# Kernel tuning notes

Hardware: AMD Instinct MI355X
Metric: run time of the kernel (lower is better)

## Reference

```python
import jax, jax.numpy as jnp
import numpy as np

N = 16384          # total nodes (128 graphs x 128 ops)
G = 128            # number of graphs
NPG = N // G       # nodes per graph
DIN = 64           # op_input_dim
H = 64             # hidden_dim
BN_EPS = 1e-5


def setup_inputs() -> dict:
    key = jax.random.key(0)
    ks = jax.random.split(key, 16)
    x = jax.random.normal(ks[0], (N, DIN), dtype=jnp.float32)
    # sparse-ish 0/1 adjacency stored dense (as torch.mm path expects); add self-loops so degrees > 0
    u = jax.random.uniform(ks[1], (N, N), dtype=jnp.float32)
    adj = jnp.maximum((u < 0.004).astype(jnp.float32), jnp.eye(N, dtype=jnp.float32))
    # graph_pool: [G, N] average-pooling matrix (block rows of 1/NPG)
    rows = jnp.repeat(jnp.arange(G), NPG)
    graph_pool = jnp.zeros((G, N), jnp.float32).at[rows, jnp.arange(N)].set(1.0 / NPG)
    s = 0.05
    params = {}
    dims_in = [DIN, H]
    for l in range(2):
        d_in = dims_in[l]
        params[f"W1_{l}"] = jax.random.normal(ks[2 + 6 * l], (d_in, H), jnp.float32) * s
        params[f"b1_{l}"] = jnp.zeros((H,), jnp.float32)
        params[f"g1_{l}"] = jnp.ones((H,), jnp.float32)
        params[f"be1_{l}"] = jnp.zeros((H,), jnp.float32)
        params[f"W2_{l}"] = jax.random.normal(ks[3 + 6 * l], (H, H), jnp.float32) * s
        params[f"b2_{l}"] = jnp.zeros((H,), jnp.float32)
        params[f"g_{l}"] = jnp.ones((H,), jnp.float32)   # outer BN gamma
        params[f"be_{l}"] = jnp.zeros((H,), jnp.float32)  # outer BN beta
    return {"x": x, "adj": adj, "graph_pool": graph_pool, **params}


def _bn(h, g, b):
    # training-mode BatchNorm1d over node axis (biased var), eps=1e-5
    m = jnp.mean(h, axis=0)
    v = jnp.var(h, axis=0)
    return g * (h - m) * jax.lax.rsqrt(v + BN_EPS) + b


def _mlp(h, W1, b1, g1, be1, W2, b2):
    # 2-layer MLP: Linear -> BN -> ReLU -> Linear
    return jax.nn.relu(_bn(h @ W1 + b1, g1, be1)) @ W2 + b2


def reference(x, adj, graph_pool,
              W1_0, b1_0, g1_0, be1_0, W2_0, b2_0, g_0, be_0,
              W1_1, b1_1, g1_1, be1_1, W2_1, b2_1, g_1, be_1):
    deg = adj @ jnp.ones((adj.shape[0], 1), adj.dtype)  # [N,1]
    h = x
    layers = [
        (W1_0, b1_0, g1_0, be1_0, W2_0, b2_0, g_0, be_0),
        (W1_1, b1_1, g1_1, be1_1, W2_1, b2_1, g_1, be_1),
    ]
    for (W1, b1, g1, be1, W2, b2, g, be) in layers:
        pooled = (adj @ h) / deg                 # average neighbor aggregation
        pooled_rep = _mlp(pooled, W1, b1, g1, be1, W2, b2)
        h = jax.nn.relu(_bn(pooled_rep, g, be))
    h_nodes = h
    pooled_h = graph_pool @ h                    # [G, H] graph readout
    return (pooled_h, h_nodes)
```

## Files before the change

### kernel.cpp

```cpp
#include <hip/hip_runtime.h>
#include <hip/hip_bf16.h>
#include <stdint.h>

#define N_NODES 16384
#define GG      128
#define HD      64
#define MAXD    192
#define BN_EPS  1e-5f

typedef unsigned short u16;
typedef unsigned int   u32;
typedef unsigned long long u64;
typedef u32 u32x4 __attribute__((ext_vector_type(4)));

__device__ __forceinline__ float bf2f(u16 u) {
    union { u32 i; float f; } c; c.i = ((u32)u) << 16; return c.f;
}
__device__ __forceinline__ float ldp(const void* p, int i, int flag) {
    return flag ? ((const float*)p)[i] : bf2f(((const u16*)p)[i]);
}

__global__ __launch_bounds__(256) void k_scan_gather(
    const void* __restrict__ adjv, const void* __restrict__ xv,
    u16* __restrict__ cols, int* __restrict__ cnt,
    float* __restrict__ invdeg, float* __restrict__ pooled,
    double* __restrict__ statsD, int* __restrict__ flagp)
{
    __shared__ __align__(16) u16 sc[4][MAXD];
    const int wave = threadIdx.x >> 6, lane = threadIdx.x & 63;
    const int row = blockIdx.x * 4 + wave;
    const u32 w0 = *(const u32*)adjv;
    const int flag = ((w0 & 0xFFFFu) == 0) ? 1 : 0;
    const u64 ltmask = ((1ull << lane) - 1ull);

    const int gid = blockIdx.x * 256 + threadIdx.x;
    if (gid < 512) statsD[gid] = 0.0;
    if (gid == 0) *flagp = flag;

    u16* __restrict__ srow = sc[wave];
    int base = 0;
    if (flag) {
        const u32x4* __restrict__ arow =
            (const u32x4*)((const u32*)adjv + (size_t)row * N_NODES) + lane;
        u32x4 p0 = __builtin_nontemporal_load(arow);
        u32x4 p1 = __builtin_nontemporal_load(arow + 64);
        for (int c = 0; c < N_NODES; c += 256) {
            u32x4 raw = p0;
            p0 = p1;
            if (c + 512 < N_NODES)
                p1 = __builtin_nontemporal_load(arow + (c + 512) / 4);
            #pragma unroll
            for (int e = 0; e < 4; ++e) {
                u32 w = raw[e];
                u64 m = __ballot(w != 0);
                if (m) {
                    if (w) {
                        int p = base + __popcll(m & ltmask);
                        if (p < MAXD) srow[p] = (u16)(c + lane * 4 + e);
                    }
                    base += __popcll(m);
                }
            }
        }
    } else {
        const u32x4* __restrict__ arow =
            (const u32x4*)((const u16*)adjv + (size_t)row * N_NODES) + lane;
        u32x4 p0 = __builtin_nontemporal_load(arow);
        u32x4 p1 = __builtin_nontemporal_load(arow + 64);
        for (int c = 0; c < N_NODES; c += 512) {
            u32x4 raw = p0;
            p0 = p1;
            if (c + 1024 < N_NODES)
                p1 = __builtin_nontemporal_load(arow + (c + 1024) / 8);
            #pragma unroll
            for (int e = 0; e < 8; ++e) {
                u16 u = (u16)(raw[e >> 1] >> ((e & 1) * 16));
                u64 m = __ballot(u != 0);
                if (m) {
                    if (u) {
                        int p = base + __popcll(m & ltmask);
                        if (p < MAXD) srow[p] = (u16)(c + lane * 8 + e);
                    }
                    base += __popcll(m);
                }
            }
        }
    }
    const int n = (base < MAXD) ? base : MAXD;
    if (lane == 0) cnt[row] = n;
    __syncthreads();

    {
        u32* __restrict__ crow32 = (u32*)(cols + (size_t)row * MAXD);
        const u32* __restrict__ s32 = (const u32*)srow;
        #pragma unroll
        for (int t = lane; t < MAXD / 2; t += 64) crow32[t] = s32[t];
    }

    float acc = 0.f;
    int k = 0;
    if (flag) {
        const float* __restrict__ x = (const float*)xv;
        for (; k + 4 <= n; k += 4) {
            ushort4 j4 = *(const ushort4*)&srow[k];
            float v0 = x[(size_t)j4.x * HD + lane];
            float v1 = x[(size_t)j4.y * HD + lane];
            float v2 = x[(size_t)j4.z * HD + lane];
            float v3 = x[(size_t)j4.w * HD + lane];
            acc += (v0 + v1) + (v2 + v3);
        }
        for (; k < n; ++k) acc += x[(size_t)srow[k] * HD + lane];
    } else {
        const u16* __restrict__ x = (const u16*)xv;
        for (; k + 4 <= n; k += 4) {
            ushort4 j4 = *(const ushort4*)&srow[k];
            float v0 = bf2f(x[(size_t)j4.x * HD + lane]);
            float v1 = bf2f(x[(size_t)j4.y * HD + lane]);
            float v2 = bf2f(x[(size_t)j4.z * HD + lane]);
            float v3 = bf2f(x[(size_t)j4.w * HD + lane]);
            acc += (v0 + v1) + (v2 + v3);
        }
        for (; k < n; ++k) acc += bf2f(x[(size_t)srow[k] * HD + lane]);
    }
    float inv = 1.f / (float)n;
    pooled[(size_t)row * HD + lane] = acc * inv;
    if (lane == 0) invdeg[row] = inv;
}

template<bool AFFINE>
__global__ __launch_bounds__(256) void k_mm(
    const float* __restrict__ src, const double* __restrict__ stats,
    const void* __restrict__ g, const void* __restrict__ be,
    const void* __restrict__ W, const void* __restrict__ bias,
    float* __restrict__ dst, const int* __restrict__ flagp)
{
    __shared__ float Wf[64 * 64];
    __shared__ float S[16 * 64];
    __shared__ float ac[128];
    const int tid = threadIdx.x;
    const int flag = *flagp;
    if (AFFINE) {
        if (tid < 64) {
            double m = stats[tid] * (1.0 / N_NODES);
            double v = stats[64 + tid] * (1.0 / N_NODES) - m * m;
            float A = ldp(g, tid, flag) / sqrtf((float)v + BN_EPS);
            ac[tid] = A;
            ac[64 + tid] = ldp(be, tid, flag) - (float)m * A;
        }
        __syncthreads();
    }
    for (int i = tid; i < 64 * 64; i += 256) Wf[i] = ldp(W, i, flag);
    const int rbase = blockIdx.x * 16;
    {
        float4 v = *(const float4*)&src[(size_t)rbase * 64 + tid * 4];
        if (AFFINE) {
            const int f0 = (tid * 4) & 63;
            v.x = fmaxf(fmaf(ac[f0 + 0], v.x, ac[64 + f0 + 0]), 0.f);
            v.y = fmaxf(fmaf(ac[f0 + 1], v.y, ac[64 + f0 + 1]), 0.f);
            v.z = fmaxf(fmaf(ac[f0 + 2], v.z, ac[64 + f0 + 2]), 0.f);
            v.w = fmaxf(fmaf(ac[f0 + 3], v.w, ac[64 + f0 + 3]), 0.f);
        }
        *(float4*)&S[tid * 4] = v;
    }
    __syncthreads();
    const int f = tid & 63, r0 = (tid >> 6) * 4;
    const float b = ldp(bias, f, flag);
    float a0 = b, a1 = b, a2 = b, a3 = b;
    #pragma unroll
    for (int k = 0; k < 64; ++k) {
        const float wk = Wf[k * 64 + f];
        a0 = fmaf(S[(r0 + 0) * 64 + k], wk, a0);
        a1 = fmaf(S[(r0 + 1) * 64 + k], wk, a1);
        a2 = fmaf(S[(r0 + 2) * 64 + k], wk, a2);
        a3 = fmaf(S[(r0 + 3) * 64 + k], wk, a3);
    }
    dst[(size_t)(rbase + r0 + 0) * 64 + f] = a0;
    dst[(size_t)(rbase + r0 + 1) * 64 + f] = a1;
    dst[(size_t)(rbase + r0 + 2) * 64 + f] = a2;
    dst[(size_t)(rbase + r0 + 3) * 64 + f] = a3;
}

__global__ __launch_bounds__(256) void k_stats(
    const float* __restrict__ src, double* __restrict__ statsOut)
{
    __shared__ double shs[256];
    __shared__ double shq[256];
    const int tid = threadIdx.x;
    const int f = tid & 63, rsub = tid >> 6;
    const int rbase = blockIdx.x * 64;
    double s = 0.0, q = 0.0;
    for (int r = rsub; r < 64; r += 4) {
        float v = src[(size_t)(rbase + r) * 64 + f];
        s += (double)v;
        q += (double)v * (double)v;
    }
    shs[tid] = s; shq[tid] = q;
    __syncthreads();
    if (tid < 64) {
        double S = shs[tid] + shs[64 + tid] + shs[128 + tid] + shs[192 + tid];
        double Q = shq[tid] + shq[64 + tid] + shq[128 + tid] + shq[192 + tid];
        atomicAdd(&statsOut[tid], S);
        atomicAdd(&statsOut[64 + tid], Q);
    }
}

__global__ __launch_bounds__(256) void k_bnrelu(
    const float* __restrict__ src, const double* __restrict__ stats,
    const void* __restrict__ g, const void* __restrict__ be,
    float* __restrict__ dst, const int* __restrict__ flagp)
{
    __shared__ float ac[128];
    const int tid = threadIdx.x;
    const int flag = *flagp;
    if (tid < 64) {
        double m = stats[tid] * (1.0 / N_NODES);
        double v = stats[64 + tid] * (1.0 / N_NODES) - m * m;
        float A = ldp(g, tid, flag) / sqrtf((float)v + BN_EPS);
        ac[tid] = A;
        ac[64 + tid] = ldp(be, tid, flag) - (float)m * A;
    }
    __syncthreads();
    const size_t idx = ((size_t)blockIdx.x * 256 + tid) * 4;
    const int f0 = (int)(idx & 63);
    float4 t = *(const float4*)&src[idx];
    const float4 A4 = *(const float4*)&ac[f0];
    const float4 C4 = *(const float4*)&ac[64 + f0];
    float4 r;
    r.x = fmaxf(fmaf(A4.x, t.x, C4.x), 0.f);
    r.y = fmaxf(fmaf(A4.y, t.y, C4.y), 0.f);
    r.z = fmaxf(fmaf(A4.z, t.z, C4.z), 0.f);
    r.w = fmaxf(fmaf(A4.w, t.w, C4.w), 0.f);
    *(float4*)&dst[idx] = r;
}

__global__ __launch_bounds__(256) void k_spmm(
    const float* __restrict__ t, const double* __restrict__ stats,
    const void* __restrict__ g, const void* __restrict__ be,
    const u16* __restrict__ cols, const int* __restrict__ cnt,
    const float* __restrict__ invdeg, float* __restrict__ pooled,
    const int* __restrict__ flagp)
{
    const int wave = threadIdx.x >> 6, lane = threadIdx.x & 63;
    const int row = blockIdx.x * 4 + wave;
    const int flag = *flagp;
    double md = stats[lane] * (1.0 / N_NODES);
    double vd = stats[64 + lane] * (1.0 / N_NODES) - md * md;
    const float A = ldp(g, lane, flag) / sqrtf((float)vd + BN_EPS);
    const float C = ldp(be, lane, flag) - (float)md * A;

    const u16* __restrict__ crow = cols + (size_t)row * MAXD;
    const int n = cnt[row];
    float acc = 0.f;
    int k = 0;
    for (; k + 4 <= n; k += 4) {
        ushort4 j4 = *(const ushort4*)&crow[k];
        float v0 = t[(size_t)j4.x * HD + lane];
        float v1 = t[(size_t)j4.y * HD + lane];
        float v2 = t[(size_t)j4.z * HD + lane];
        float v3 = t[(size_t)j4.w * HD + lane];
        acc += fmaxf(fmaf(A, v0, C), 0.f);
        acc += fmaxf(fmaf(A, v1, C), 0.f);
        acc += fmaxf(fmaf(A, v2, C), 0.f);
        acc += fmaxf(fmaf(A, v3, C), 0.f);
    }
    for (; k < n; ++k) {
        float vv = t[(size_t)crow[k] * HD + lane];
        acc += fmaxf(fmaf(A, vv, C), 0.f);
    }
    pooled[(size_t)row * HD + lane] = acc * invdeg[row];
}

__global__ __launch_bounds__(1024) void k_pool(
    const void* __restrict__ gpv, const float* __restrict__ h,
    float* __restrict__ out, const int* __restrict__ flagp)
{
    __shared__ float red[16 * 64];
    const int g = blockIdx.x;
    const int wave = threadIdx.x >> 6, lane = threadIdx.x & 63;
    const int flag = *flagp;
    float acc = 0.f;
    const int jb0 = wave * (N_NODES / 16);
    if (flag) {
        const float* __restrict__ grow = (const float*)gpv + (size_t)g * N_NODES;
        for (int jb = jb0; jb < jb0 + N_NODES / 16; jb += 4) {
            float4 raw = *(const float4*)(grow + jb);
            if (raw.x != 0.f) acc += raw.x * h[(size_t)(jb + 0) * HD + lane];
            if (raw.y != 0.f) acc += raw.y * h[(size_t)(jb + 1) * HD + lane];
            if (raw.z != 0.f) acc += raw.z * h[(size_t)(jb + 2) * HD + lane];
            if (raw.w != 0.f) acc += raw.w * h[(size_t)(jb + 3) * HD + lane];
        }
    } else {
        const u16* __restrict__ grow = (const u16*)gpv + (size_t)g * N_NODES;
        for (int jb = jb0; jb < jb0 + N_NODES / 16; jb += 8) {
            uint4 raw = *(const uint4*)(grow + jb);
            const u32 w[4] = {raw.x, raw.y, raw.z, raw.w};
            #pragma unroll
            for (int e = 0; e < 8; ++e) {
                u16 u = (u16)(w[e >> 1] >> ((e & 1) * 16));
                if (u) acc += bf2f(u) * h[(size_t)(jb + e) * HD + lane];
            }
        }
    }
    red[wave * 64 + lane] = acc;
    __syncthreads();
    if (wave == 0) {
        float s = 0.f;
        #pragma unroll
        for (int w2 = 0; w2 < 16; ++w2) s += red[w2 * 64 + lane];
        out[g * 64 + lane] = s;
    }
}

extern "C" void kernel_launch(void* const* d_in, const int* in_sizes, int n_in,
                              void* d_out, int out_size, void* d_ws, size_t ws_size,
                              hipStream_t stream)
{
    const void* x    = d_in[0];
    const void* adj  = d_in[1];
    const void* gp   = d_in[2];
    const void* W1_0 = d_in[3];
    const void* b1_0 = d_in[4];
    const void* g1_0 = d_in[5];
    const void* be1_0= d_in[6];
    const void* W2_0 = d_in[7];
    const void* b2_0 = d_in[8];
    const void* g_0  = d_in[9];
    const void* be_0 = d_in[10];
    const void* W1_1 = d_in[11];
    const void* b1_1 = d_in[12];
    const void* g1_1 = d_in[13];
    const void* be1_1= d_in[14];
    const void* W2_1 = d_in[15];
    const void* b2_1 = d_in[16];
    const void* g_1  = d_in[17];
    const void* be_1 = d_in[18];

    char* ws = (char*)d_ws;
    float*  P      = (float*) (ws);
    float*  A      = (float*) (ws + (4u  << 20));
    float*  B      = (float*) (ws + (8u  << 20));
    u16*    cols   = (u16*)   (ws + (12u << 20));
    int*    cnt    = (int*)   (ws + (18u << 20));
    float*  invdeg = (float*) (ws + (18u << 20) + 65536);
    double* sd     = (double*)(ws + (18u << 20) + 131072);
    int*    flag   = (int*)   (ws + (18u << 20) + 131072 + 4096);

    float* out_pool  = (float*)d_out;
    float* out_nodes = (float*)d_out + GG * HD;

    const int EB = (N_NODES * HD / 4) / 256;

    k_scan_gather<<<N_NODES / 4, 256, 0, stream>>>(adj, x, cols, cnt,
                                                   invdeg, P, sd, flag);

    k_mm<false><<<N_NODES / 16, 256, 0, stream>>>(P, nullptr, nullptr, nullptr,
                                                  W1_0, b1_0, A, flag);
    k_stats<<<256, 256, 0, stream>>>(A, sd + 0);
    k_mm<true><<<N_NODES / 16, 256, 0, stream>>>(A, sd + 0, g1_0, be1_0,
                                                 W2_0, b2_0, P, flag);
    k_stats<<<256, 256, 0, stream>>>(P, sd + 128);
    k_spmm<<<N_NODES / 4, 256, 0, stream>>>(P, sd + 128, g_0, be_0,
                                            cols, cnt, invdeg, B, flag);
    k_mm<false><<<N_NODES / 16, 256, 0, stream>>>(B, nullptr, nullptr, nullptr,
                                                  W1_1, b1_1, A, flag);
    k_stats<<<256, 256, 0, stream>>>(A, sd + 256);
    k_mm<true><<<N_NODES / 16, 256, 0, stream>>>(A, sd + 256, g1_1, be1_1,
                                                 W2_1, b2_1, P, flag);
    k_stats<<<256, 256, 0, stream>>>(P, sd + 384);
    k_bnrelu<<<EB, 256, 0, stream>>>(P, sd + 384, g_1, be_1, out_nodes, flag);
    k_pool<<<GG, 1024, 0, stream>>>(gp, out_nodes, out_pool, flag);
}
```

Baseline: 1.604 ms.

## Fuse BN statistics into matmul epilogue and merge final BN-ReLU with pooling

Each matmul kernel now accumulates per-feature sum and sum of squares in its epilogue. It spreads the double atomics across 16 slots, which consumers sum when they build the BN affine. This removes the four separate stats kernels and their extra reads of the intermediate activations. The final BN-ReLU and graph pooling become one launch, with pooling blocks recomputing BN-ReLU from the pre-BN buffer so they no longer wait on the written node output. The cost is more atomics and shared memory in each matmul block, plus slot reductions in every consumer.

```diff
diff --git a/kernel.cpp b/kernel.cpp
--- a/kernel.cpp
+++ b/kernel.cpp
@@ -7,6 +7,7 @@
 #define HD      64
 #define MAXD    192
 #define BN_EPS  1e-5f
+#define NSLOT   16
 
 typedef unsigned short u16;
 typedef unsigned int   u32;
@@ -34,7 +35,7 @@
     const u64 ltmask = ((1ull << lane) - 1ull);
 
     const int gid = blockIdx.x * 256 + threadIdx.x;
-    if (gid < 512) statsD[gid] = 0.0;
+    if (gid < 4 * NSLOT * 128) statsD[gid] = 0.0;
     if (gid == 0) *flagp = flag;
 
     u16* __restrict__ srow = sc[wave];
@@ -129,20 +130,29 @@
 
 template<bool AFFINE>
 __global__ __launch_bounds__(256) void k_mm(
-    const float* __restrict__ src, const double* __restrict__ stats,
+    const float* __restrict__ src, const double* __restrict__ statsIn,
     const void* __restrict__ g, const void* __restrict__ be,
     const void* __restrict__ W, const void* __restrict__ bias,
-    float* __restrict__ dst, const int* __restrict__ flagp)
+    float* __restrict__ dst, double* __restrict__ statsOut,
+    const int* __restrict__ flagp)
 {
     __shared__ float Wf[64 * 64];
     __shared__ float S[16 * 64];
     __shared__ float ac[128];
+    __shared__ double shs[256];
+    __shared__ double shq[256];
     const int tid = threadIdx.x;
     const int flag = *flagp;
     if (AFFINE) {
         if (tid < 64) {
-            double m = stats[tid] * (1.0 / N_NODES);
-            double v = stats[64 + tid] * (1.0 / N_NODES) - m * m;
+            double ss = 0.0, qq = 0.0;
+            #pragma unroll
+            for (int s2 = 0; s2 < NSLOT; ++s2) {
+                ss += statsIn[s2 * 128 + tid];
+                qq += statsIn[s2 * 128 + 64 + tid];
+            }
+            double m = ss * (1.0 / N_NODES);
+            double v = qq * (1.0 / N_NODES) - m * m;
             float A = ldp(g, tid, flag) / sqrtf((float)v + BN_EPS);
             ac[tid] = A;
             ac[64 + tid] = ldp(be, tid, flag) - (float)m * A;
@@ -178,75 +188,47 @@
     dst[(size_t)(rbase + r0 + 1) * 64 + f] = a1;
     dst[(size_t)(rbase + r0 + 2) * 64 + f] = a2;
     dst[(size_t)(rbase + r0 + 3) * 64 + f] = a3;
-}
-
-__global__ __launch_bounds__(256) void k_stats(
-    const float* __restrict__ src, double* __restrict__ statsOut)
-{
-    __shared__ double shs[256];
-    __shared__ double shq[256];
-    const int tid = threadIdx.x;
-    const int f = tid & 63, rsub = tid >> 6;
-    const int rbase = blockIdx.x * 64;
-    double s = 0.0, q = 0.0;
-    for (int r = rsub; r < 64; r += 4) {
-        float v = src[(size_t)(rbase + r) * 64 + f];
-        s += (double)v;
-        q += (double)v * (double)v;
-    }
-    shs[tid] = s; shq[tid] = q;
+
+    shs[tid] = (double)a0 + (double)a1 + (double)a2 + (double)a3;
+    shq[tid] = (double)a0 * a0 + (double)a1 * a1
+             + (double)a2 * a2 + (double)a3 * a3;
     __syncthreads();
     if (tid < 64) {
-        double S = shs[tid] + shs[64 + tid] + shs[128 + tid] + shs[192 + tid];
-        double Q = shq[tid] + shq[64 + tid] + shq[128 + tid] + shq[192 + tid];
-        atomicAdd(&statsOut[tid], S);
-        atomicAdd(&statsOut[64 + tid], Q);
-    }
-}
-
-__global__ __launch_bounds__(256) void k_bnrelu(
-    const float* __restrict__ src, const double* __restrict__ stats,
-    const void* __restrict__ g, const void* __restrict__ be,
-    float* __restrict__ dst, const int* __restrict__ flagp)
-{
-    __shared__ float ac[128];
-    const int tid = threadIdx.x;
-    const int flag = *flagp;
-    if (tid < 64) {
-        double m = stats[tid] * (1.0 / N_NODES);
-        double v = stats[64 + tid] * (1.0 / N_NODES) - m * m;
-        float A = ldp(g, tid, flag) / sqrtf((float)v + BN_EPS);
-        ac[tid] = A;
-        ac[64 + tid] = ldp(be, tid, flag) - (float)m * A;
-    }
-    __syncthreads();
-    const size_t idx = ((size_t)blockIdx.x * 256 + tid) * 4;
-    const int f0 = (int)(idx & 63);
-    float4 t = *(const float4*)&src[idx];
-    const float4 A4 = *(const float4*)&ac[f0];
-    const float4 C4 = *(const float4*)&ac[64 + f0];
-    float4 r;
-    r.x = fmaxf(fmaf(A4.x, t.x, C4.x), 0.f);
-    r.y = fmaxf(fmaf(A4.y, t.y, C4.y), 0.f);
-    r.z = fmaxf(fmaf(A4.z, t.z, C4.z), 0.f);
-    r.w = fmaxf(fmaf(A4.w, t.w, C4.w), 0.f);
-    *(float4*)&dst[idx] = r;
+        double S2 = shs[tid] + shs[64 + tid] + shs[128 + tid] + shs[192 + tid];
+        double Q2 = shq[tid] + shq[64 + tid] + shq[128 + tid] + shq[192 + tid];
+        double* so = statsOut + (blockIdx.x & (NSLOT - 1)) * 128;
+        atomicAdd(&so[tid], S2);
+        atomicAdd(&so[64 + tid], Q2);
+    }
 }
 
 __global__ __launch_bounds__(256) void k_spmm(
-    const float* __restrict__ t, const double* __restrict__ stats,
+    const float* __restrict__ t, const double* __restrict__ statsIn,
     const void* __restrict__ g, const void* __restrict__ be,
     const u16* __restrict__ cols, const int* __restrict__ cnt,
     const float* __restrict__ invdeg, float* __restrict__ pooled,
     const int* __restrict__ flagp)
 {
-    const int wave = threadIdx.x >> 6, lane = threadIdx.x & 63;
+    __shared__ float ac[128];
+    const int tid = threadIdx.x;
+    const int wave = tid >> 6, lane = tid & 63;
     const int row = blockIdx.x * 4 + wave;
     const int flag = *flagp;
-    double md = stats[lane] * (1.0 / N_NODES);
-    double vd = stats[64 + lane] * (1.0 / N_NODES) - md * md;
-    const float A = ldp(g, lane, flag) / sqrtf((float)vd + BN_EPS);
-    const float C = ldp(be, lane, flag) - (float)md * A;
+    if (tid < 64) {
+        double ss = 0.0, qq = 0.0;
+        #pragma unroll
+        for (int s2 = 0; s2 < NSLOT; ++s2) {
+            ss += statsIn[s2 * 128 + tid];
+            qq += statsIn[s2 * 128 + 64 + tid];
+        }
+        double m = ss * (1.0 / N_NODES);
+        double v = qq * (1.0 / N_NODES) - m * m;
+        float A = ldp(g, tid, flag) / sqrtf((float)v + BN_EPS);
+        ac[tid] = A;
+        ac[64 + tid] = ldp(be, tid, flag) - (float)m * A;
+    }
+    __syncthreads();
+    const float A = ac[lane], C = ac[64 + lane];
 
     const u16* __restrict__ crow = cols + (size_t)row * MAXD;
     const int n = cnt[row];
@@ -270,44 +252,85 @@
     pooled[(size_t)row * HD + lane] = acc * invdeg[row];
 }
 
-__global__ __launch_bounds__(1024) void k_pool(
-    const void* __restrict__ gpv, const float* __restrict__ h,
-    float* __restrict__ out, const int* __restrict__ flagp)
-{
+__global__ __launch_bounds__(1024) void k_bnrelu_pool(
+    const float* __restrict__ P, const double* __restrict__ statsIn,
+    const void* __restrict__ g, const void* __restrict__ be,
+    const void* __restrict__ gpv, float* __restrict__ out_nodes,
+    float* __restrict__ out_pool, const int* __restrict__ flagp)
+{
+    __shared__ float ac[128];
     __shared__ float red[16 * 64];
-    const int g = blockIdx.x;
-    const int wave = threadIdx.x >> 6, lane = threadIdx.x & 63;
+    const int tid = threadIdx.x;
     const int flag = *flagp;
-    float acc = 0.f;
-    const int jb0 = wave * (N_NODES / 16);
-    if (flag) {
-        const float* __restrict__ grow = (const float*)gpv + (size_t)g * N_NODES;
-        for (int jb = jb0; jb < jb0 + N_NODES / 16; jb += 4) {
-            float4 raw = *(const float4*)(grow + jb);
-            if (raw.x != 0.f) acc += raw.x * h[(size_t)(jb + 0) * HD + lane];
-            if (raw.y != 0.f) acc += raw.y * h[(size_t)(jb + 1) * HD + lane];
-            if (raw.z != 0.f) acc += raw.z * h[(size_t)(jb + 2) * HD + lane];
-            if (raw.w != 0.f) acc += raw.w * h[(size_t)(jb + 3) * HD + lane];
-        }
+    if (tid < 64) {
+        double ss = 0.0, qq = 0.0;
+        #pragma unroll
+        for (int s2 = 0; s2 < NSLOT; ++s2) {
+            ss += statsIn[s2 * 128 + tid];
+            qq += statsIn[s2 * 128 + 64 + tid];
+        }
+        double m = ss * (1.0 / N_NODES);
+        double v = qq * (1.0 / N_NODES) - m * m;
+        float A = ldp(g, tid, flag) / sqrtf((float)v + BN_EPS);
+        ac[tid] = A;
+        ac[64 + tid] = ldp(be, tid, flag) - (float)m * A;
+    }
+    __syncthreads();
+
+    if (blockIdx.x < 256) {
+        const size_t idx = ((size_t)blockIdx.x * 1024 + tid) * 4;
+        const int f0 = (int)(idx & 63);
+        float4 t = *(const float4*)&P[idx];
+        const float4 A4 = *(const float4*)&ac[f0];
+        const float4 C4 = *(const float4*)&ac[64 + f0];
+        float4 r;
+        r.x = fmaxf(fmaf(A4.x, t.x, C4.x), 0.f);
+        r.y = fmaxf(fmaf(A4.y, t.y, C4.y), 0.f);
+        r.z = fmaxf(fmaf(A4.z, t.z, C4.z), 0.f);
+        r.w = fmaxf(fmaf(A4.w, t.w, C4.w), 0.f);
+        *(float4*)&out_nodes[idx] = r;
     } else {
-        const u16* __restrict__ grow = (const u16*)gpv + (size_t)g * N_NODES;
-        for (int jb = jb0; jb < jb0 + N_NODES / 16; jb += 8) {
-            uint4 raw = *(const uint4*)(grow + jb);
-            const u32 w[4] = {raw.x, raw.y, raw.z, raw.w};
+        const int gidx = blockIdx.x - 256;
+        const int wave = tid >> 6, lane = tid & 63;
+        const float A = ac[lane], C = ac[64 + lane];
+        float acc = 0.f;
+        const int jb0 = wave * (N_NODES / 16);
+        if (flag) {
+            const float* __restrict__ grow =
+                (const float*)gpv + (size_t)gidx * N_NODES;
+            for (int jb = jb0; jb < jb0 + N_NODES / 16; jb += 4) {
+                float4 raw = *(const float4*)(grow + jb);
+                if (raw.x != 0.f)
+                    acc += raw.x * fmaxf(fmaf(A, P[(size_t)(jb + 0) * HD + lane], C), 0.f);
+                if (raw.y != 0.f)
+                    acc += raw.y * fmaxf(fmaf(A, P[(size_t)(jb + 1) * HD + lane], C), 0.f);
+                if (raw.z != 0.f)
+                    acc += raw.z * fmaxf(fmaf(A, P[(size_t)(jb + 2) * HD + lane], C), 0.f);
+                if (raw.w != 0.f)
+                    acc += raw.w * fmaxf(fmaf(A, P[(size_t)(jb + 3) * HD + lane], C), 0.f);
+            }
+        } else {
+            const u16* __restrict__ grow =
+                (const u16*)gpv + (size_t)gidx * N_NODES;
+            for (int jb = jb0; jb < jb0 + N_NODES / 16; jb += 8) {
+                uint4 raw = *(const uint4*)(grow + jb);
+                const u32 w[4] = {raw.x, raw.y, raw.z, raw.w};
+                #pragma unroll
+                for (int e = 0; e < 8; ++e) {
+                    u16 u = (u16)(w[e >> 1] >> ((e & 1) * 16));
+                    if (u)
+                        acc += bf2f(u) * fmaxf(fmaf(A, P[(size_t)(jb + e) * HD + lane], C), 0.f);
+                }
+            }
+        }
+        red[wave * 64 + lane] = acc;
+        __syncthreads();
+        if (wave == 0) {
+            float s = 0.f;
             #pragma unroll
-            for (int e = 0; e < 8; ++e) {
-                u16 u = (u16)(w[e >> 1] >> ((e & 1) * 16));
-                if (u) acc += bf2f(u) * h[(size_t)(jb + e) * HD + lane];
-            }
-        }
-    }
-    red[wave * 64 + lane] = acc;
-    __syncthreads();
-    if (wave == 0) {
-        float s = 0.f;
-        #pragma unroll
-        for (int w2 = 0; w2 < 16; ++w2) s += red[w2 * 64 + lane];
-        out[g * 64 + lane] = s;
+            for (int w2 = 0; w2 < 16; ++w2) s += red[w2 * 64 + lane];
+            out_pool[gidx * 64 + lane] = s;
+        }
     }
 }
 
@@ -343,30 +366,29 @@
     int*    cnt    = (int*)   (ws + (18u << 20));
     float*  invdeg = (float*) (ws + (18u << 20) + 65536);
     double* sd     = (double*)(ws + (18u << 20) + 131072);
-    int*    flag   = (int*)   (ws + (18u << 20) + 131072 + 4096);
+    int*    flag   = (int*)   (ws + (18u << 20) + 131072 + 65536);
 
     float* out_pool  = (float*)d_out;
     float* out_nodes = (float*)d_out + GG * HD;
 
-    const int EB = (N_NODES * HD / 4) / 256;
+    double* st0 = sd + 0 * NSLOT * 128;
+    double* st1 = sd + 1 * NSLOT * 128;
+    double* st2 = sd + 2 * NSLOT * 128;
+    double* st3 = sd + 3 * NSLOT * 128;
 
     k_scan_gather<<<N_NODES / 4, 256, 0, stream>>>(adj, x, cols, cnt,
                                                    invdeg, P, sd, flag);
 
     k_mm<false><<<N_NODES / 16, 256, 0, stream>>>(P, nullptr, nullptr, nullptr,
-                                                  W1_0, b1_0, A, flag);
-    k_stats<<<256, 256, 0, stream>>>(A, sd + 0);
-    k_mm<true><<<N_NODES / 16, 256, 0, stream>>>(A, sd + 0, g1_0, be1_0,
-                                                 W2_0, b2_0, P, flag);
-    k_stats<<<256, 256, 0, stream>>>(P, sd + 128);
-    k_spmm<<<N_NODES / 4, 256, 0, stream>>>(P, sd + 128, g_0, be_0,
+                                                  W1_0, b1_0, A, st0, flag);
+    k_mm<true><<<N_NODES / 16, 256, 0, stream>>>(A, st0, g1_0, be1_0,
+                                                 W2_0, b2_0, P, st1, flag);
+    k_spmm<<<N_NODES / 4, 256, 0, stream>>>(P, st1, g_0, be_0,
                                             cols, cnt, invdeg, B, flag);
     k_mm<false><<<N_NODES / 16, 256, 0, stream>>>(B, nullptr, nullptr, nullptr,
-                                                  W1_1, b1_1, A, flag);
-    k_stats<<<256, 256, 0, stream>>>(A, sd + 256);
-    k_mm<true><<<N_NODES / 16, 256, 0, stream>>>(A, sd + 256, g1_1, be1_1,
-                                                 W2_1, b2_1, P, flag);
-    k_stats<<<256, 256, 0, stream>>>(P, sd + 384);
-    k_bnrelu<<<EB, 256, 0, stream>>>(P, sd + 384, g_1, be_1, out_nodes, flag);
-    k_pool<<<GG, 1024, 0, stream>>>(gp, out_nodes, out_pool, flag);
-}
+                                                  W1_1, b1_1, A, st2, flag);
+    k_mm<true><<<N_NODES / 16, 256, 0, stream>>>(A, st2, g1_1, be1_1,
+                                                 W2_1, b2_1, P, st3, flag);
+    k_bnrelu_pool<<<256 + GG, 1024, 0, stream>>>(P, st3, g_1, be_1, gp,
+                                                 out_nodes, out_pool, flag);
+}
```

After: 1.544 ms. -3.7%, faster.
